# Optimization experiments

Measured on AMD Instinct MI355X. Metric: run time of the kernel, lower is better.

## Reference

```python
import jax, jax.numpy as jnp
import numpy as np

B, FEAT_DIM, NUM_BANDS = 64, 512, 8
H_VAL, W_VAL = 1024, 1024


def setup_inputs() -> dict:
    key = jax.random.key(0)
    k1, k2, k3 = jax.random.split(key, 3)
    freq_feat = jax.random.normal(k1, (B, FEAT_DIM), dtype=jnp.float32)
    w = jax.random.normal(k2, (NUM_BANDS, FEAT_DIM), dtype=jnp.float32) * 0.05
    b = jax.random.normal(k3, (NUM_BANDS,), dtype=jnp.float32) * 0.05
    return {"freq_feat": freq_feat, "w": w, "b": b, "H": H_VAL, "W": W_VAL}


def reference(freq_feat, w, b, H, W):
    # MLP: Linear(feat_dim -> num_bands) + Softmax over bands
    logits = freq_feat @ w.T + b                      # [B, nb]
    band_weights = jax.nn.softmax(logits, axis=1)     # [B, nb]
    nb = band_weights.shape[1]

    # Radial frequency grid, shape [H, W//2+1]
    u = jnp.fft.rfftfreq(W).astype(freq_feat.dtype)
    v = jnp.fft.fftfreq(H).astype(freq_feat.dtype)
    v_grid, u_grid = jnp.meshgrid(v, u, indexing='ij')
    radius = jnp.sqrt(u_grid ** 2 + v_grid ** 2)
    max_r = radius.max()

    # Band membership masks for all bands at once: [nb, H, W//2+1]
    i = jnp.arange(nb, dtype=freq_feat.dtype)
    lower = max_r * (i / nb)
    upper = max_r * ((i + 1.0) / nb)
    masks = ((radius[None] >= lower[:, None, None]) &
             (radius[None] < upper[:, None, None])).astype(freq_feat.dtype)

    # Weighted sum over bands -> [B, 1, H, W//2+1]
    freq_mask = jnp.einsum('bn,nhw->bhw', band_weights, masks)
    return freq_mask[:, None, :, :]
```

## Files before the change

### kernel.cpp

```cpp
#include <hip/hip_runtime.h>
#include <math.h>

#define NB     8
#define BATCH  64
#define FEAT   512
#define HGT    1024
#define WHALF  513
#define PIX    (HGT * WHALF)
#define TOTAL  (BATCH * PIX)

#define MAX_R  0x1.6A09E6p-1f

typedef float vfloat4 __attribute__((ext_vector_type(4)));

__device__ __forceinline__ int band_of(int p) {
    const int h  = p / WHALF;
    const int wp = p - h * WHALF;
    const float u = (float)wp * 0.0009765625f;
    const int hv  = (h >= 512) ? (h - 1024) : h;
    const float v = (float)hv * 0.0009765625f;
    const float r = sqrtf(fmaf(u, u, v * v));

    int j = (int)(r * (8.0f / MAX_R));
    if (j > 8) j = 8;
    const float lo = MAX_R * ((float)j * 0.125f);
    if (r < lo) {
        --j;
    } else if (j < 8) {
        const float hi = MAX_R * ((float)(j + 1) * 0.125f);
        if (r >= hi) ++j;
    }
    return j;
}

__global__ void __launch_bounds__(256)
prep_kernel(const float* __restrict__ ff,
            const float* __restrict__ w,
            const float* __restrict__ bias,
            float* __restrict__ bw,
            unsigned char* __restrict__ band) {
    const int t = threadIdx.x;

    if (blockIdx.x >= BATCH) {
        const int p = (blockIdx.x - BATCH) * 1024 + t * 4;
        uchar4 o;
        o.x = (unsigned char)band_of(p + 0);
        o.y = (unsigned char)band_of(p + 1);
        o.z = (unsigned char)band_of(p + 2);
        o.w = (unsigned char)band_of(p + 3);
        *reinterpret_cast<uchar4*>(band + p) = o;
        return;
    }

    const int b = blockIdx.x;
    float part[NB];
#pragma unroll
    for (int n = 0; n < NB; ++n) part[n] = 0.0f;

    for (int k = t; k < FEAT; k += 256) {
        const float f = ff[b * FEAT + k];
#pragma unroll
        for (int n = 0; n < NB; ++n) part[n] += f * w[n * FEAT + k];
    }

#pragma unroll
    for (int n = 0; n < NB; ++n) {
#pragma unroll
        for (int off = 32; off > 0; off >>= 1)
            part[n] += __shfl_down(part[n], off);
    }

    __shared__ float red[4][NB];
    const int wave = t >> 6, lane = t & 63;
    if (lane == 0) {
#pragma unroll
        for (int n = 0; n < NB; ++n) red[wave][n] = part[n];
    }
    __syncthreads();

    if (t == 0) {
        float logit[NB], m = -1e30f;
#pragma unroll
        for (int n = 0; n < NB; ++n) {
            logit[n] = red[0][n] + red[1][n] + red[2][n] + red[3][n] + bias[n];
            m = fmaxf(m, logit[n]);
        }
        float s = 0.0f;
#pragma unroll
        for (int n = 0; n < NB; ++n) { logit[n] = expf(logit[n] - m); s += logit[n]; }
        const float inv = 1.0f / s;
#pragma unroll
        for (int n = 0; n < NB; ++n) bw[b * NB + n] = logit[n] * inv;
    }
}

__global__ void __launch_bounds__(256)
out_kernel(const float* __restrict__ bw,
           const unsigned char* __restrict__ band,
           float* __restrict__ out) {
    __shared__ float sbw[BATCH * 9];
    for (int i = threadIdx.x; i < BATCH * 9; i += 256) {
        const int b = i / 9, j = i - b * 9;
        sbw[i] = (j < NB) ? bw[b * NB + j] : 0.0f;
    }
    __syncthreads();

    const int chunk = blockIdx.x >> 3;
    const int bg    = blockIdx.x & 7;
    const int p     = chunk * 1024 + (int)threadIdx.x * 4;

    const uchar4 j4 = *reinterpret_cast<const uchar4*>(band + p);

    float* o = out + (size_t)(bg * 8) * PIX + p;
#pragma unroll
    for (int i = 0; i < 8; ++i) {
        const float* row = sbw + (bg * 8 + i) * 9;
        vfloat4 v;
        v.x = row[j4.x];
        v.y = row[j4.y];
        v.z = row[j4.z];
        v.w = row[j4.w];
        __builtin_nontemporal_store(v, reinterpret_cast<vfloat4*>(o));
        o += PIX;
    }
}

__global__ void __launch_bounds__(256)
out_fused_kernel(const float* __restrict__ bw, float* __restrict__ out) {
    __shared__ float sbw[BATCH * 9];
    for (int i = threadIdx.x; i < BATCH * 9; i += 256) {
        const int b = i / 9, j = i - b * 9;
        sbw[i] = (j < NB) ? bw[b * NB + j] : 0.0f;
    }
    __syncthreads();

    const int nq = TOTAL / 4;
    const int stride = gridDim.x * blockDim.x;
    for (int q = blockIdx.x * blockDim.x + threadIdx.x; q < nq; q += stride) {
        const int base = q * 4;
        const int b = base / PIX;
        const int p = base - b * PIX;
        const float* row = sbw + b * 9;
        float4 o;
        o.x = row[band_of(p + 0)];
        o.y = row[band_of(p + 1)];
        o.z = row[band_of(p + 2)];
        o.w = row[band_of(p + 3)];
        reinterpret_cast<float4*>(out)[q] = o;
    }
}

extern "C" void kernel_launch(void* const* d_in, const int* in_sizes, int n_in,
                              void* d_out, int out_size, void* d_ws, size_t ws_size,
                              hipStream_t stream) {
    const float* ff   = (const float*)d_in[0];
    const float* w    = (const float*)d_in[1];
    const float* bias = (const float*)d_in[2];
    float* out = (float*)d_out;

    float* bw = (float*)d_ws;
    unsigned char* band = (unsigned char*)d_ws + 2048;

    if (ws_size >= 2048 + (size_t)PIX) {
        prep_kernel<<<BATCH + PIX / 1024, 256, 0, stream>>>(ff, w, bias, bw, band);
        out_kernel<<<(PIX / 1024) * 8, 256, 0, stream>>>(bw, band, out);
    } else {
        prep_kernel<<<BATCH, 256, 0, stream>>>(ff, w, bias, bw, band);
        out_fused_kernel<<<2048, 256, 0, stream>>>(bw, out);
    }
}
```

Measured before the change: 150.1 us.

## Fuse MLP softmax and band lookup into a single output kernel

Merges the prep and output kernels into one launch. Each block recomputes the linear layer and softmax for its 8 batch rows, with the dot products split across threads and the softmax reductions done with shuffles. Each block also computes band indices inline instead of reading a precomputed byte map. This removes a kernel launch and the workspace round trip. In exchange, every block redundantly reads 8 feature rows and the weights (about 32KB, mostly from cache), which adds latency before the stores begin.

```diff
diff --git a/kernel.cpp b/kernel.cpp
--- a/kernel.cpp
+++ b/kernel.cpp
@@ -4,11 +4,8 @@
 #define NB     8
 #define BATCH  64
 #define FEAT   512
-#define HGT    1024
 #define WHALF  513
-#define PIX    (HGT * WHALF)
-#define TOTAL  (BATCH * PIX)
-
+#define PIX    (1024 * 513)
 #define MAX_R  0x1.6A09E6p-1f
 
 typedef float vfloat4 __attribute__((ext_vector_type(4)));
@@ -34,119 +31,66 @@
 }
 
 __global__ void __launch_bounds__(256)
-prep_kernel(const float* __restrict__ ff,
-            const float* __restrict__ w,
-            const float* __restrict__ bias,
-            float* __restrict__ bw,
-            unsigned char* __restrict__ band) {
-    const int t = threadIdx.x;
+fused_kernel(const float* __restrict__ ff,
+             const float* __restrict__ w,
+             const float* __restrict__ bias,
+             float* __restrict__ out) {
+    const int t     = threadIdx.x;
+    const int chunk = blockIdx.x >> 3;
+    const int bg    = blockIdx.x & 7;
 
-    if (blockIdx.x >= BATCH) {
-        const int p = (blockIdx.x - BATCH) * 1024 + t * 4;
-        uchar4 o;
-        o.x = (unsigned char)band_of(p + 0);
-        o.y = (unsigned char)band_of(p + 1);
-        o.z = (unsigned char)band_of(p + 2);
-        o.w = (unsigned char)band_of(p + 3);
-        *reinterpret_cast<uchar4*>(band + p) = o;
-        return;
-    }
+    __shared__ float red[4][64];
+    __shared__ float sbw[NB * 9];
 
-    const int b = blockIdx.x;
-    float part[NB];
+    {
+        const int pair = t & 63;
+        const int q    = t >> 6;
+        const int bl   = pair >> 3, n = pair & 7;
+        const float* fr = ff + (size_t)(bg * 8 + bl) * FEAT + q * 128;
+        const float* wr = w  + (size_t)n * FEAT + q * 128;
+        float acc = 0.0f;
 #pragma unroll
-    for (int n = 0; n < NB; ++n) part[n] = 0.0f;
-
-    for (int k = t; k < FEAT; k += 256) {
-        const float f = ff[b * FEAT + k];
-#pragma unroll
-        for (int n = 0; n < NB; ++n) part[n] += f * w[n * FEAT + k];
-    }
-
-#pragma unroll
-    for (int n = 0; n < NB; ++n) {
-#pragma unroll
-        for (int off = 32; off > 0; off >>= 1)
-            part[n] += __shfl_down(part[n], off);
-    }
-
-    __shared__ float red[4][NB];
-    const int wave = t >> 6, lane = t & 63;
-    if (lane == 0) {
-#pragma unroll
-        for (int n = 0; n < NB; ++n) red[wave][n] = part[n];
+        for (int k = 0; k < 128; k += 4) {
+            const float4 a = *reinterpret_cast<const float4*>(fr + k);
+            const float4 c = *reinterpret_cast<const float4*>(wr + k);
+            acc += a.x * c.x + a.y * c.y + a.z * c.z + a.w * c.w;
+        }
+        red[q][pair] = acc;
     }
     __syncthreads();
 
-    if (t == 0) {
-        float logit[NB], m = -1e30f;
+    if (t < 64) {
+        const int bl = t >> 3, n = t & 7;
+        float logit = red[0][t] + red[1][t] + red[2][t] + red[3][t] + bias[n];
+        float m = logit;
 #pragma unroll
-        for (int n = 0; n < NB; ++n) {
-            logit[n] = red[0][n] + red[1][n] + red[2][n] + red[3][n] + bias[n];
-            m = fmaxf(m, logit[n]);
-        }
-        float s = 0.0f;
+        for (int s = 1; s < 8; s <<= 1) m = fmaxf(m, __shfl_xor(m, s));
+        const float e = expf(logit - m);
+        float sum = e;
 #pragma unroll
-        for (int n = 0; n < NB; ++n) { logit[n] = expf(logit[n] - m); s += logit[n]; }
-        const float inv = 1.0f / s;
-#pragma unroll
-        for (int n = 0; n < NB; ++n) bw[b * NB + n] = logit[n] * inv;
-    }
-}
-
-__global__ void __launch_bounds__(256)
-out_kernel(const float* __restrict__ bw,
-           const unsigned char* __restrict__ band,
-           float* __restrict__ out) {
-    __shared__ float sbw[BATCH * 9];
-    for (int i = threadIdx.x; i < BATCH * 9; i += 256) {
-        const int b = i / 9, j = i - b * 9;
-        sbw[i] = (j < NB) ? bw[b * NB + j] : 0.0f;
+        for (int s = 1; s < 8; s <<= 1) sum += __shfl_xor(sum, s);
+        sbw[bl * 9 + n] = e / sum;
+        if (n == 0) sbw[bl * 9 + 8] = 0.0f;
     }
     __syncthreads();
 
-    const int chunk = blockIdx.x >> 3;
-    const int bg    = blockIdx.x & 7;
-    const int p     = chunk * 1024 + (int)threadIdx.x * 4;
-
-    const uchar4 j4 = *reinterpret_cast<const uchar4*>(band + p);
+    const int p  = chunk * 1024 + t * 4;
+    const int j0 = band_of(p + 0);
+    const int j1 = band_of(p + 1);
+    const int j2 = band_of(p + 2);
+    const int j3 = band_of(p + 3);
 
     float* o = out + (size_t)(bg * 8) * PIX + p;
 #pragma unroll
     for (int i = 0; i < 8; ++i) {
-        const float* row = sbw + (bg * 8 + i) * 9;
+        const float* row = sbw + i * 9;
         vfloat4 v;
-        v.x = row[j4.x];
-        v.y = row[j4.y];
-        v.z = row[j4.z];
-        v.w = row[j4.w];
+        v.x = row[j0];
+        v.y = row[j1];
+        v.z = row[j2];
+        v.w = row[j3];
         __builtin_nontemporal_store(v, reinterpret_cast<vfloat4*>(o));
         o += PIX;
-    }
-}
-
-__global__ void __launch_bounds__(256)
-out_fused_kernel(const float* __restrict__ bw, float* __restrict__ out) {
-    __shared__ float sbw[BATCH * 9];
-    for (int i = threadIdx.x; i < BATCH * 9; i += 256) {
-        const int b = i / 9, j = i - b * 9;
-        sbw[i] = (j < NB) ? bw[b * NB + j] : 0.0f;
-    }
-    __syncthreads();
-
-    const int nq = TOTAL / 4;
-    const int stride = gridDim.x * blockDim.x;
-    for (int q = blockIdx.x * blockDim.x + threadIdx.x; q < nq; q += stride) {
-        const int base = q * 4;
-        const int b = base / PIX;
-        const int p = base - b * PIX;
-        const float* row = sbw + b * 9;
-        float4 o;
-        o.x = row[band_of(p + 0)];
-        o.y = row[band_of(p + 1)];
-        o.z = row[band_of(p + 2)];
-        o.w = row[band_of(p + 3)];
-        reinterpret_cast<float4*>(out)[q] = o;
     }
 }
 
@@ -158,14 +102,6 @@
     const float* bias = (const float*)d_in[2];
     float* out = (float*)d_out;
 
-    float* bw = (float*)d_ws;
-    unsigned char* band = (unsigned char*)d_ws + 2048;
-
-    if (ws_size >= 2048 + (size_t)PIX) {
-        prep_kernel<<<BATCH + PIX / 1024, 256, 0, stream>>>(ff, w, bias, bw, band);
-        out_kernel<<<(PIX / 1024) * 8, 256, 0, stream>>>(bw, band, out);
-    } else {
-        prep_kernel<<<BATCH, 256, 0, stream>>>(ff, w, bias, bw, band);
-        out_fused_kernel<<<2048, 256, 0, stream>>>(bw, out);
-    }
+    (void)d_ws; (void)ws_size;
+    fused_kernel<<<513 * 8, 256, 0, stream>>>(ff, w, bias, out);
 }
```

New measurement: 205.4 us. 1.37x slower.
